# Kernel tuning notes

Measured on AMD Instinct MI355X. Metric: run time of the kernel, lower is better.

Reference implementation:

```python
import jax, jax.numpy as jnp
import numpy as np

B, N, E, H = 8, 512, 256, 8
DK = E // H
DIST_BAR = (0.3, 0.7, 1e10)  # init dist_bar + [1e10] appended in forward
NEG = -1e10


def setup_inputs() -> dict:
    key = jax.random.key(0)
    ks = jax.random.split(key, 24)
    s = 0.02
    inp = {
        'query': jax.random.normal(ks[0], (B, N, E), jnp.float32),
        'key':   jax.random.normal(ks[1], (B, N, E), jnp.float32),
        'value': jax.random.normal(ks[2], (B, N, E), jnp.float32),
        'dist':  jax.random.uniform(ks[3], (B, N, N), jnp.float32),
        'mask':  jax.random.randint(ks[4], (B, N, N), 0, 2).astype(jnp.int32),
        # 4 linears (q, k, v, out), stored as [in, out] for x @ W
        'Wq': jax.random.normal(ks[5], (E, E)) * s, 'bq': jnp.zeros((E,)),
        'Wk': jax.random.normal(ks[6], (E, E)) * s, 'bk': jnp.zeros((E,)),
        'Wv': jax.random.normal(ks[7], (E, E)) * s, 'bv': jnp.zeros((E,)),
        'Wo': jax.random.normal(ks[8], (E, E)) * s, 'bo': jnp.zeros((E,)),
        # cnn: Conv2d(1,H,1) -> ReLU -> Conv2d(H,H,1); 1x1 convs = per-pixel linear maps
        'cw1': jax.random.normal(ks[9], (H,)) * s,     'cb1': jnp.zeros((H,)),
        'cw2': jax.random.normal(ks[10], (H, H)) * s,  'cb2': jnp.zeros((H,)),
        # scale_linear: Linear(3E, E) -> ReLU -> Linear(E, E)
        'Ws1': jax.random.normal(ks[11], (3 * E, E)) * s, 'bs1': jnp.zeros((E,)),
        'Ws2': jax.random.normal(ks[12], (E, E)) * s,     'bs2': jnp.zeros((E,)),
    }
    return inp


def reference(query, key, value, dist, mask,
              Wq, bq, Wk, bk, Wv, bv, Wo, bo,
              cw1, cb1, cw2, cb2, Ws1, bs1, Ws2, bs2):
    def heads(x, W, b):  # [B,N,E] -> [B,H,N,DK]
        return (x @ W + b).reshape(B, N, H, DK).transpose(0, 2, 1, 3)

    q, k, v = heads(query, Wq, bq), heads(key, Wk, bk), heads(value, Wv, bv)
    d4 = dist[:, None]  # [B,1,N,N]
    # 1x1 conv stack: [B,1,N,N] -> [B,H,N,N]
    c1 = jax.nn.relu(d4 * cw1[None, :, None, None] + cb1[None, :, None, None])
    dist_conv = jnp.einsum('oi,bijk->bojk', cw2, c1) + cb2[None, :, None, None]

    scores = jnp.einsum('bhqd,bhkd->bhqk', q, k) / np.sqrt(DK).astype(np.float32)
    scores = scores * dist_conv
    scores = jnp.where(mask[:, None] == 0, NEG, scores)

    outs = []
    for bar in DIST_BAR:
        dm = d4 < bar                       # [B,1,N,N] bool
        dm = dm.at[:, :, 0, :].set(True).at[:, :, :, 0].set(True)
        s = jnp.where(dm, scores, NEG)
        p = jax.nn.softmax(s, axis=-1)      # [B,H,N,N]
        o = jnp.einsum('bhqk,bhkd->bhqd', p, v)
        o = o.transpose(0, 2, 1, 3).reshape(B, N, E)
        outs.append(o @ Wo + bo)
    x = jnp.concatenate(outs, axis=-1)      # [B,N,3E]
    h1 = jax.nn.relu(x @ Ws1 + bs1)
    return h1 @ Ws2 + bs2                   # [B,N,E]
```

## Files before the change

kernel.cpp:

```cpp
#include <hip/hip_runtime.h>
#include <math.h>

typedef _Float16 h16;
typedef __attribute__((ext_vector_type(4))) _Float16 h16x4;
typedef __attribute__((ext_vector_type(8))) _Float16 h16x8;
typedef __attribute__((ext_vector_type(4))) float f32x4;
typedef unsigned long long u64t;
typedef unsigned int u32t;
typedef unsigned char u8t;

__global__ __launch_bounds__(256) void prep_k(
    const float* __restrict__ Wq, const float* __restrict__ Wk,
    const float* __restrict__ Wv, const float* __restrict__ Ws2,
    const float* __restrict__ Ws1, const float* __restrict__ bo,
    const float* __restrict__ bs1,
    const float* __restrict__ cw1, const float* __restrict__ cb1,
    const float* __restrict__ cw2, const float* __restrict__ cb2,
    h16* __restrict__ WT, float* __restrict__ bcombP,
    float* __restrict__ tthr, float* __restrict__ fLUT)
{
    const int bid = blockIdx.x;
    __shared__ float T[32][33];
    if (bid < 448) {
        const int z = bid >> 6, idx = bid & 63;
        const float* in = (z == 0) ? Wq : (z == 1) ? Wk : (z == 2) ? Wv :
                          (z == 3) ? Ws2 : (Ws1 + (size_t)(z - 4) * 65536);
        h16* out = WT + (size_t)z * 65536;
        const int t = threadIdx.x, tx = t & 31, ty = t >> 5;
        const int r0 = (idx >> 3) * 32, c0 = (idx & 7) * 32;
        #pragma unroll
        for (int i = 0; i < 4; ++i)
            T[ty + i * 8][tx] = in[(size_t)(r0 + ty + i * 8) * 256 + c0 + tx];
        __syncthreads();
        #pragma unroll
        for (int i = 0; i < 4; ++i)
            out[(size_t)(c0 + ty + i * 8) * 256 + r0 + tx] = (h16)T[tx][ty + i * 8];
    } else if (bid < 464) {
        const int z = bid - 448;
        const int j = threadIdx.x;
        float acc = (z == 0) ? bs1[j] : 0.f;
        const int r0 = z * 48;
        #pragma unroll 4
        for (int r = r0; r < r0 + 48; ++r)
            acc = fmaf(bo[r & 255], Ws1[(size_t)r * 256 + j], acc);
        bcombP[z * 256 + j] = acc;
    } else {
        const int t = threadIdx.x;
        const float INVS = 0.17677669529663687f;
        float tv[8]; int zu[8];
        #pragma unroll
        for (int u = 0; u < 8; ++u) {
            const float w = cw1[u];
            zu[u] = (w == 0.f) ? 1 : 0;
            tv[u] = zu[u] ? 3.0e38f : (-cb1[u] / w);
        }
        if (t < 8) tthr[t] = tv[t];
        if (t < 72) {
            const int h = t & 7, jj = t >> 3;
            int rank[8];
            #pragma unroll
            for (int u = 0; u < 8; ++u) {
                int rk = 0;
                #pragma unroll
                for (int v = 0; v < 8; ++v)
                    rk += ((tv[v] < tv[u]) || (tv[v] == tv[u] && v < u)) ? 1 : 0;
                rank[u] = rk;
            }
            float slope = 0.f, inter = cb2[h];
            #pragma unroll
            for (int u = 0; u < 8; ++u) {
                const float c2 = cw2[h * 8 + u];
                if (zu[u]) {
                    inter += c2 * fmaxf(cb1[u], 0.f);
                } else {
                    const bool act = (cw1[u] > 0.f) ? (rank[u] < jj) : (rank[u] >= jj);
                    if (act) {
                        slope = fmaf(c2, cw1[u], slope);
                        inter = fmaf(c2, cb1[u], inter);
                    }
                }
            }
            float2 e; e.x = INVS * slope; e.y = INVS * inter;
            ((float2*)fLUT)[jj * 8 + h] = e;
        }
    }
}

__global__ __launch_bounds__(256) void qkvw_k(
    const float* __restrict__ Xq, const float* __restrict__ Xk,
    const float* __restrict__ Xv, const float* __restrict__ Wo,
    const h16* __restrict__ WT,
    const float* __restrict__ bq, const float* __restrict__ bk,
    const float* __restrict__ bv,
    h16* __restrict__ qb, h16* __restrict__ kb, h16* __restrict__ vbT,
    h16* __restrict__ WbigT)
{
    const int bid = blockIdx.x;
    const float* A; const h16* Bt; const float* bias = nullptr;
    int mode, row0, col0, sgm = 0;
    if (bid < 768) {
        const int z = bid >> 8, r = bid & 255;
        row0 = (r & 63) * 64; col0 = (r >> 6) * 64;
        A = (z == 0) ? Xq : (z == 1) ? Xk : Xv;
        Bt = WT + (size_t)z * 65536;
        bias = (z == 0) ? bq : (z == 1) ? bk : bv;
        mode = z;
    } else {
        const int r = bid - 768;
        sgm = r >> 4; const int tt = r & 15;
        row0 = (tt >> 2) * 64; col0 = (tt & 3) * 64;
        A = Wo; Bt = WT + (size_t)(4 + sgm) * 65536; mode = 3;
    }

    __shared__ __align__(16) h16 As[2][64][40];
    __shared__ __align__(16) h16 Bs[2][64][40];
    const int t = threadIdx.x, w = t >> 6, lane = t & 63;
    const int Q = lane >> 4, n = lane & 15;
    const int sr = t >> 2, sc = (t & 3) * 8;

    auto ldA = [&](int k0) -> h16x8 {
        const float* ap = A + (size_t)(row0 + sr) * 256 + k0 + sc;
        float4 f0 = *(const float4*)ap;
        float4 f1 = *(const float4*)(ap + 4);
        h16x8 hv;
        hv[0] = (h16)f0.x; hv[1] = (h16)f0.y; hv[2] = (h16)f0.z; hv[3] = (h16)f0.w;
        hv[4] = (h16)f1.x; hv[5] = (h16)f1.y; hv[6] = (h16)f1.z; hv[7] = (h16)f1.w;
        return hv;
    };
    auto ldB = [&](int k0) -> h16x8 {
        return *(const h16x8*)(Bt + (size_t)(col0 + sr) * 256 + k0 + sc);
    };

    {
        h16x8 a0 = ldA(0), b0 = ldB(0);
        *(h16x8*)&As[0][sr][sc] = a0;
        *(h16x8*)&Bs[0][sr][sc] = b0;
    }
    __syncthreads();

    f32x4 acc4[4];
    #pragma unroll
    for (int c = 0; c < 4; ++c) acc4[c] = (f32x4){0.f, 0.f, 0.f, 0.f};

    for (int it = 0; it < 8; ++it) {
        const int cur = it & 1;
        h16x8 arN, brN;
        if (it < 7) { arN = ldA(32 * (it + 1)); brN = ldB(32 * (it + 1)); }
        h16x8 af = *(const h16x8*)&As[cur][w * 16 + n][Q * 8];
        #pragma unroll
        for (int cg = 0; cg < 4; ++cg) {
            h16x8 bf = *(const h16x8*)&Bs[cur][cg * 16 + n][Q * 8];
            acc4[cg] = __builtin_amdgcn_mfma_f32_16x16x32_f16(af, bf, acc4[cg], 0, 0, 0);
        }
        if (it < 7) {
            *(h16x8*)&As[cur ^ 1][sr][sc] = arN;
            *(h16x8*)&Bs[cur ^ 1][sr][sc] = brN;
        }
        __syncthreads();
    }

    if (mode < 2) {
        h16* out = mode ? kb : qb;
        #pragma unroll
        for (int cg = 0; cg < 4; ++cg) {
            const float bvv = bias[col0 + cg * 16 + n];
            #pragma unroll
            for (int r = 0; r < 4; ++r)
                out[(size_t)(row0 + w * 16 + 4 * Q + r) * 256 + col0 + cg * 16 + n] =
                    (h16)(acc4[cg][r] + bvv);
        }
    } else if (mode == 2) {
        const int bb = row0 >> 9;
        #pragma unroll
        for (int cg = 0; cg < 4; ++cg) {
            const float bvv = bias[col0 + cg * 16 + n];
            const int col = col0 + cg * 16 + n;
            #pragma unroll
            for (int r = 0; r < 4; ++r) {
                const int m = row0 + w * 16 + 4 * Q + r;
                vbT[((size_t)(bb * 256 + col)) * 512 + (m & 511)] = (h16)(acc4[cg][r] + bvv);
            }
        }
    } else {
        #pragma unroll
        for (int cg = 0; cg < 4; ++cg) {
            const int col = col0 + cg * 16 + n;
            #pragma unroll
            for (int r = 0; r < 4; ++r)
                WbigT[(size_t)col * 768 + sgm * 256 + row0 + w * 16 + 4 * Q + r] =
                    (h16)acc4[cg][r];
        }
    }
}

template<int OUT16RELU>
__global__ __launch_bounds__(256) void hgemm32_k(
    const h16* __restrict__ A, const h16* __restrict__ Bt,
    const float* __restrict__ bias, void* __restrict__ outv, int K, int nbp)
{
    __shared__ __align__(16) h16 As[2][32][72];
    __shared__ __align__(16) h16 Bs[2][64][72];
    const int t = threadIdx.x, w = t >> 6, lane = t & 63;
    const int Q = lane >> 4, n = lane & 15;
    const int row0 = blockIdx.x * 32, col0 = blockIdx.y * 64;
    const int r16 = (w & 1) * 16, c32 = (w >> 1) * 32;
    const int asr = t >> 3, asc = (t & 7) * 8;
    const int bsr = t >> 2, bsc = (t & 3) * 16;

    auto ldA = [&](int k0) -> h16x8 {
        return *(const h16x8*)(A + (size_t)(row0 + asr) * K + k0 + asc);
    };
    auto ldB0 = [&](int k0) -> h16x8 {
        return *(const h16x8*)(Bt + (size_t)(col0 + bsr) * K + k0 + bsc);
    };
    auto ldB1 = [&](int k0) -> h16x8 {
        return *(const h16x8*)(Bt + (size_t)(col0 + bsr) * K + k0 + bsc + 8);
    };

    {
        h16x8 a0 = ldA(0), b0 = ldB0(0), b1 = ldB1(0);
        *(h16x8*)&As[0][asr][asc] = a0;
        *(h16x8*)&Bs[0][bsr][bsc] = b0;
        *(h16x8*)&Bs[0][bsr][bsc + 8] = b1;
    }
    __syncthreads();

    f32x4 acc2[2];
    acc2[0] = (f32x4){0.f, 0.f, 0.f, 0.f};
    acc2[1] = (f32x4){0.f, 0.f, 0.f, 0.f};
    const int iters = K >> 6;

    for (int it = 0; it < iters; ++it) {
        const int cur = it & 1;
        h16x8 arN, brN0, brN1;
        if (it + 1 < iters) {
            arN = ldA(64 * (it + 1));
            brN0 = ldB0(64 * (it + 1));
            brN1 = ldB1(64 * (it + 1));
        }
        #pragma unroll
        for (int kh = 0; kh < 2; ++kh) {
            h16x8 af = *(const h16x8*)&As[cur][r16 + n][kh * 32 + Q * 8];
            #pragma unroll
            for (int cg = 0; cg < 2; ++cg) {
                h16x8 bf = *(const h16x8*)&Bs[cur][c32 + cg * 16 + n][kh * 32 + Q * 8];
                acc2[cg] = __builtin_amdgcn_mfma_f32_16x16x32_f16(af, bf, acc2[cg], 0, 0, 0);
            }
        }
        if (it + 1 < iters) {
            *(h16x8*)&As[cur ^ 1][asr][asc] = arN;
            *(h16x8*)&Bs[cur ^ 1][bsr][bsc] = brN0;
            *(h16x8*)&Bs[cur ^ 1][bsr][bsc + 8] = brN1;
        }
        __syncthreads();
    }

    #pragma unroll
    for (int cg = 0; cg < 2; ++cg) {
        const int col = col0 + c32 + cg * 16 + n;
        float bv = bias[col];
        for (int p = 1; p < nbp; ++p) bv += bias[p * 256 + col];
        #pragma unroll
        for (int r = 0; r < 4; ++r) {
            const int row = row0 + r16 + 4 * Q + r;
            if (OUT16RELU)
                ((h16*)outv)[(size_t)row * 256 + col] = (h16)fmaxf(acc2[cg][r] + bv, 0.f);
            else
                ((float*)outv)[(size_t)row * 256 + col] = acc2[cg][r] + bv;
        }
    }
}

__global__ __launch_bounds__(256, 2) void attn_k(
    const h16* __restrict__ qb, const h16* __restrict__ kb,
    const h16* __restrict__ vbT,
    const float* __restrict__ dist, const int* __restrict__ mask,
    const float* __restrict__ tthr, const float* __restrict__ fLUT,
    h16* __restrict__ OB)
{
    const int bx = blockIdx.x, b = bx >> 5, q0 = (bx & 31) * 16;
    const int hg = blockIdx.y;
    const int t = threadIdx.x, w = t >> 6, lane = t & 63;
    const int Q = lane >> 4, n = lane & 15;
    const int h = hg * 4 + w;

    __shared__ __align__(16) h16 Ft[2][16][66][4];
    __shared__ __align__(16) u8t Cd[2][16][72];
    __shared__ __align__(16) h16 Sx[4][16][72];
    __shared__ __align__(8)  float2 lutS[4][9];

    float th[8];
    #pragma unroll
    for (int u = 0; u < 8; ++u) th[u] = tthr[u];
    if (t < 36) {
        const int hh = t / 9, j = t - hh * 9;
        lutS[hh][j] = ((const float2*)fLUT)[j * 8 + hg * 4 + hh];
    }
    __syncthreads();

    const h16x8 aq =
        *(const h16x8*)(qb + ((size_t)(b * 512 + q0 + n)) * 256 + h * 32 + Q * 8);

    const f32x4 z4 = {0.f, 0.f, 0.f, 0.f};
    f32x4 acc[3][2];
    #pragma unroll
    for (int s = 0; s < 3; ++s) { acc[s][0] = z4; acc[s][1] = z4; }
    float mprev = -3e38f;
    float lsum[3] = {0.f, 0.f, 0.f};

    const int scol = lane;

    auto stage = [&](int buf, int kkb, const float* dp, const int* mp) {
        #pragma unroll
        for (int i = 0; i < 4; ++i) {
            const int row = w + 4 * i;
            const float d = dp[i];
            int idx = 0;
            #pragma unroll
            for (int u = 0; u < 8; ++u) idx += (d > th[u]) ? 1 : 0;
            const bool fr = ((q0 + row) == 0) || ((kkb + scol) == 0);
            const bool keep = (mp[i] != 0);
            const u32t code = (keep && (fr || d < 0.3f) ? 1u : 0u)
                            | (keep && (fr || d < 0.7f) ? 2u : 0u)
                            | (keep ? 4u : 0u);
            Cd[buf][row][scol] = (u8t)code;
            h16x4 fv;
            #pragma unroll
            for (int hh = 0; hh < 4; ++hh) {
                const float2 si = lutS[hh][idx];
                fv[hh] = (h16)fmaf(d, si.x, si.y);
            }
            *(h16x4*)&Ft[buf][row][scol][0] = fv;
        }
    };

    float dv[4]; int mkv[4];
    #pragma unroll
    for (int i = 0; i < 4; ++i) {
        const size_t off = ((size_t)(b * 512 + q0 + w + 4 * i)) * 512 + scol;
        dv[i] = dist[off]; mkv[i] = mask[off];
    }
    h16x8 kf[4], vf[4];
    #pragma unroll
    for (int cg = 0; cg < 4; ++cg)
        kf[cg] = *(const h16x8*)(kb + ((size_t)(b * 512 + cg * 16 + n)) * 256 + h * 32 + Q * 8);
    #pragma unroll
    for (int nh = 0; nh < 2; ++nh)
        #pragma unroll
        for (int k2 = 0; k2 < 2; ++k2)
            vf[nh * 2 + k2] = *(const h16x8*)(
                vbT + ((size_t)((b * 8 + h) * 32 + nh * 16 + n)) * 512 + k2 * 32 + Q * 8);
    stage(0, 0, dv, mkv);
    __syncthreads();

    for (int kc = 0; kc < 8; ++kc) {
        const int cur = kc & 1, kk0 = kc * 64;

        float dN[4]; int mkN[4]; h16x8 kfN[4], vfN[4];
        if (kc < 7) {
            const int kn = kk0 + 64;
            #pragma unroll
            for (int i = 0; i < 4; ++i) {
                const size_t off = ((size_t)(b * 512 + q0 + w + 4 * i)) * 512 + kn + scol;
                dN[i] = dist[off]; mkN[i] = mask[off];
            }
            #pragma unroll
            for (int cg = 0; cg < 4; ++cg)
                kfN[cg] = *(const h16x8*)(
                    kb + ((size_t)(b * 512 + kn + cg * 16 + n)) * 256 + h * 32 + Q * 8);
            #pragma unroll
            for (int nh = 0; nh < 2; ++nh)
                #pragma unroll
                for (int k2 = 0; k2 < 2; ++k2)
                    vfN[nh * 2 + k2] = *(const h16x8*)(
                        vbT + ((size_t)((b * 8 + h) * 32 + nh * 16 + n)) * 512
                            + kn + k2 * 32 + Q * 8);
        }

        f32x4 s4[4];
        #pragma unroll
        for (int cg = 0; cg < 4; ++cg)
            s4[cg] = __builtin_amdgcn_mfma_f32_16x16x32_f16(aq, kf[cg], z4, 0, 0, 0);

        #pragma unroll
        for (int cg = 0; cg < 4; ++cg)
            #pragma unroll
            for (int r = 0; r < 4; ++r) {
                const float f = (float)Ft[cur][4 * Q + r][cg * 16 + n][w];
                Sx[w][4 * Q + r][cg * 16 + n] = (h16)(s4[cg][r] * f);
            }
        __builtin_amdgcn_wave_barrier();

        const u64t cd0 = *(const u64t*)&Cd[cur][n][Q * 8];
        const u64t cd1 = *(const u64t*)&Cd[cur][n][32 + Q * 8];
        float sv[16];
        {
            h16x8 s0 = *(const h16x8*)&Sx[w][n][Q * 8];
            h16x8 s1 = *(const h16x8*)&Sx[w][n][32 + Q * 8];
            #pragma unroll
            for (int j = 0; j < 8; ++j) { sv[j] = (float)s0[j]; sv[8 + j] = (float)s1[j]; }
        }
        float cm = -3e38f;
        #pragma unroll
        for (int i = 0; i < 16; ++i) {
            const u32t cc = (u32t)((i < 8 ? cd0 : cd1) >> (8 * (i & 7))) & 7u;
            cm = fmaxf(cm, (cc & 4u) ? sv[i] : -3e38f);
        }
        cm = fmaxf(cm, __shfl_xor(cm, 16));
        cm = fmaxf(cm, __shfl_xor(cm, 32));
        const float mnew = fmaxf(mprev, cm);
        const float alphaA = __expf(mprev - mnew);
        mprev = mnew;

        #pragma unroll
        for (int r = 0; r < 4; ++r) {
            const float aR = __shfl(alphaA, 4 * Q + r);
            #pragma unroll
            for (int s = 0; s < 3; ++s) { acc[s][0][r] *= aR; acc[s][1][r] *= aR; }
        }

        h16x8 pf[3][2];
        float l0 = 0.f, l1 = 0.f, l2 = 0.f;
        #pragma unroll
        for (int i = 0; i < 16; ++i) {
            const u32t cc = (u32t)((i < 8 ? cd0 : cd1) >> (8 * (i & 7))) & 7u;
            const float e = __expf(sv[i] - mnew);
            const float p0 = (cc & 1u) ? e : 0.f;
            const float p1 = (cc & 2u) ? e : 0.f;
            const float p2 = (cc & 4u) ? e : 0.f;
            l0 += p0; l1 += p1; l2 += p2;
            pf[0][i >> 3][i & 7] = (h16)p0;
            pf[1][i >> 3][i & 7] = (h16)p1;
            pf[2][i >> 3][i & 7] = (h16)p2;
        }
        lsum[0] = lsum[0] * alphaA + l0;
        lsum[1] = lsum[1] * alphaA + l1;
        lsum[2] = lsum[2] * alphaA + l2;

        #pragma unroll
        for (int k2 = 0; k2 < 2; ++k2)
            #pragma unroll
            for (int nh = 0; nh < 2; ++nh)
                #pragma unroll
                for (int s = 0; s < 3; ++s)
                    acc[s][nh] = __builtin_amdgcn_mfma_f32_16x16x32_f16(
                        pf[s][k2], vf[nh * 2 + k2], acc[s][nh], 0, 0, 0);

        if (kc < 7) {
            stage(cur ^ 1, kk0 + 64, dN, mkN);
            #pragma unroll
            for (int i = 0; i < 4; ++i) { kf[i] = kfN[i]; vf[i] = vfN[i]; dv[i] = dN[i]; mkv[i] = mkN[i]; }
        }
        __syncthreads();
    }

    float lrow[3];
    #pragma unroll
    for (int s = 0; s < 3; ++s) {
        float lv = lsum[s];
        lv += __shfl_xor(lv, 16);
        lv += __shfl_xor(lv, 32);
        lrow[s] = lv;
    }
    #pragma unroll
    for (int s = 0; s < 3; ++s) {
        #pragma unroll
        for (int r = 0; r < 4; ++r) {
            const float il = 1.0f / __shfl(lrow[s], 4 * Q + r);
            const size_t row = (size_t)(b * 512 + q0 + 4 * Q + r);
            h16* op = OB + row * 768 + s * 256 + h * 32 + n;
            op[0]  = (h16)(acc[s][0][r] * il);
            op[16] = (h16)(acc[s][1][r] * il);
        }
    }
}

extern "C" void kernel_launch(void* const* d_in, const int* in_sizes, int n_in,
                              void* d_out, int out_size, void* d_ws, size_t ws_size,
                              hipStream_t stream)
{
    const float* query = (const float*)d_in[0];
    const float* key   = (const float*)d_in[1];
    const float* value = (const float*)d_in[2];
    const float* dist  = (const float*)d_in[3];
    const int*   mask  = (const int*)d_in[4];
    const float* Wq = (const float*)d_in[5];  const float* bq = (const float*)d_in[6];
    const float* Wk = (const float*)d_in[7];  const float* bk = (const float*)d_in[8];
    const float* Wv = (const float*)d_in[9];  const float* bv = (const float*)d_in[10];
    const float* Wo = (const float*)d_in[11]; const float* bo = (const float*)d_in[12];
    const float* cw1 = (const float*)d_in[13]; const float* cb1 = (const float*)d_in[14];
    const float* cw2 = (const float*)d_in[15]; const float* cb2 = (const float*)d_in[16];
    const float* Ws1 = (const float*)d_in[17]; const float* bs1 = (const float*)d_in[18];
    const float* Ws2 = (const float*)d_in[19]; const float* bs2 = (const float*)d_in[20];

    h16* qb    = (h16*)d_ws;
    h16* kb    = qb + 1048576;
    h16* vbT   = kb + 1048576;
    h16* OB    = vbT + 1048576;
    h16* h1    = OB + 3145728;
    h16* WT    = h1 + 1048576;
    h16* WbigT = WT + 458752;
    float* bcombP = (float*)(WbigT + 196608);
    float* tthr   = bcombP + 4096;
    float* fLUT   = tthr + 8;

    prep_k<<<dim3(465), 256, 0, stream>>>(Wq, Wk, Wv, Ws2, Ws1, bo, bs1,
                                          cw1, cb1, cw2, cb2, WT, bcombP, tthr, fLUT);

    qkvw_k<<<dim3(816), 256, 0, stream>>>(query, key, value, Wo, WT,
                                          bq, bk, bv, qb, kb, vbT, WbigT);

    attn_k<<<dim3(256, 2), 256, 0, stream>>>(qb, kb, vbT, dist, mask,
                                             tthr, fLUT, OB);

    hgemm32_k<1><<<dim3(128, 4), 256, 0, stream>>>(OB, WbigT, bcombP, h1, 768, 16);
    hgemm32_k<0><<<dim3(128, 4), 256, 0, stream>>>(h1, WT + 3 * 65536, bs2, d_out, 256, 1);
}
```

Measured before the change: 166.0 us.

## Merge head groups into one 8-wave attention block and pre-convert GEMM inputs to fp16

The attention kernel now uses 512-thread blocks that cover all 8 heads, so dist and mask are loaded and staged once per query tile instead of once per head group. Shared memory holds the fp16 distance plus a LUT index packed into the code byte, and the per-head conv factor is applied at softmax time rather than staged per head. Separately, prep_k converts query/key/value/Wo to fp16 into workspace, so the QKV GEMM loads fp16 directly instead of converting fp32 on the fly. This adds an extra conversion pass over the inputs and more per-element ALU work in the softmax loop. The grid also halves to 256 blocks, which may reduce occupancy.

```diff
diff --git a/kernel.cpp b/kernel.cpp
--- a/kernel.cpp
+++ b/kernel.cpp
@@ -16,8 +16,11 @@
     const float* __restrict__ bs1,
     const float* __restrict__ cw1, const float* __restrict__ cb1,
     const float* __restrict__ cw2, const float* __restrict__ cb2,
+    const float* __restrict__ Xq, const float* __restrict__ Xk,
+    const float* __restrict__ Xv, const float* __restrict__ Wo,
     h16* __restrict__ WT, float* __restrict__ bcombP,
-    float* __restrict__ tthr, float* __restrict__ fLUT)
+    float* __restrict__ tthr, float* __restrict__ fLUT,
+    h16* __restrict__ XHx, h16* __restrict__ XHw)
 {
     const int bid = blockIdx.x;
     __shared__ float T[32][33];
@@ -44,7 +47,7 @@
         for (int r = r0; r < r0 + 48; ++r)
             acc = fmaf(bo[r & 255], Ws1[(size_t)r * 256 + j], acc);
         bcombP[z * 256 + j] = acc;
-    } else {
+    } else if (bid == 464) {
         const int t = threadIdx.x;
         const float INVS = 0.17677669529663687f;
         float tv[8]; int zu[8];
@@ -83,12 +86,28 @@
             float2 e; e.x = INVS * slope; e.y = INVS * inter;
             ((float2*)fLUT)[jj * 8 + h] = e;
         }
+    } else {
+        const size_t idx = (size_t)(bid - 465) * 2048 + (size_t)threadIdx.x * 8;
+        const float* src; h16* dst;
+        if (idx < 3145728) {
+            const int z = (int)(idx >> 20);
+            src = ((z == 0) ? Xq : (z == 1) ? Xk : Xv) + (idx & 1048575);
+            dst = XHx + idx;
+        } else {
+            src = Wo + (idx - 3145728);
+            dst = XHw + (idx - 3145728);
+        }
+        float4 f0 = *(const float4*)src;
+        float4 f1 = *(const float4*)(src + 4);
+        h16x8 hv;
+        hv[0] = (h16)f0.x; hv[1] = (h16)f0.y; hv[2] = (h16)f0.z; hv[3] = (h16)f0.w;
+        hv[4] = (h16)f1.x; hv[5] = (h16)f1.y; hv[6] = (h16)f1.z; hv[7] = (h16)f1.w;
+        *(h16x8*)dst = hv;
     }
 }
 
 __global__ __launch_bounds__(256) void qkvw_k(
-    const float* __restrict__ Xq, const float* __restrict__ Xk,
-    const float* __restrict__ Xv, const float* __restrict__ Wo,
+    const h16* __restrict__ XHx, const h16* __restrict__ XHw,
     const h16* __restrict__ WT,
     const float* __restrict__ bq, const float* __restrict__ bk,
     const float* __restrict__ bv,
@@ -96,12 +115,12 @@
     h16* __restrict__ WbigT)
 {
     const int bid = blockIdx.x;
-    const float* A; const h16* Bt; const float* bias = nullptr;
+    const h16* A; const h16* Bt; const float* bias = nullptr;
     int mode, row0, col0, sgm = 0;
     if (bid < 768) {
         const int z = bid >> 8, r = bid & 255;
         row0 = (r & 63) * 64; col0 = (r >> 6) * 64;
-        A = (z == 0) ? Xq : (z == 1) ? Xk : Xv;
+        A = XHx + (size_t)z * 1048576;
         Bt = WT + (size_t)z * 65536;
         bias = (z == 0) ? bq : (z == 1) ? bk : bv;
         mode = z;
@@ -109,7 +128,7 @@
         const int r = bid - 768;
         sgm = r >> 4; const int tt = r & 15;
         row0 = (tt >> 2) * 64; col0 = (tt & 3) * 64;
-        A = Wo; Bt = WT + (size_t)(4 + sgm) * 65536; mode = 3;
+        A = XHw; Bt = WT + (size_t)(4 + sgm) * 65536; mode = 3;
     }
 
     __shared__ __align__(16) h16 As[2][64][40];
@@ -119,13 +138,7 @@
     const int sr = t >> 2, sc = (t & 3) * 8;
 
     auto ldA = [&](int k0) -> h16x8 {
-        const float* ap = A + (size_t)(row0 + sr) * 256 + k0 + sc;
-        float4 f0 = *(const float4*)ap;
-        float4 f1 = *(const float4*)(ap + 4);
-        h16x8 hv;
-        hv[0] = (h16)f0.x; hv[1] = (h16)f0.y; hv[2] = (h16)f0.z; hv[3] = (h16)f0.w;
-        hv[4] = (h16)f1.x; hv[5] = (h16)f1.y; hv[6] = (h16)f1.z; hv[7] = (h16)f1.w;
-        return hv;
+        return *(const h16x8*)(A + (size_t)(row0 + sr) * 256 + k0 + sc);
     };
     auto ldB = [&](int k0) -> h16x8 {
         return *(const h16x8*)(Bt + (size_t)(col0 + sr) * 256 + k0 + sc);
@@ -271,7 +284,7 @@
     }
 }
 
-__global__ __launch_bounds__(256, 2) void attn_k(
+__global__ __launch_bounds__(512, 2) void attn_k(
     const h16* __restrict__ qb, const h16* __restrict__ kb,
     const h16* __restrict__ vbT,
     const float* __restrict__ dist, const int* __restrict__ mask,
@@ -279,24 +292,19 @@
     h16* __restrict__ OB)
 {
     const int bx = blockIdx.x, b = bx >> 5, q0 = (bx & 31) * 16;
-    const int hg = blockIdx.y;
     const int t = threadIdx.x, w = t >> 6, lane = t & 63;
     const int Q = lane >> 4, n = lane & 15;
-    const int h = hg * 4 + w;
-
-    __shared__ __align__(16) h16 Ft[2][16][66][4];
+    const int h = w;
+
+    __shared__ __align__(16) h16 Dd[2][16][72];
     __shared__ __align__(16) u8t Cd[2][16][72];
-    __shared__ __align__(16) h16 Sx[4][16][72];
-    __shared__ __align__(8)  float2 lutS[4][9];
+    __shared__ __align__(16) h16 Sx[8][16][72];
+    __shared__ __align__(8)  float2 lutS[8][9];
 
     float th[8];
     #pragma unroll
     for (int u = 0; u < 8; ++u) th[u] = tthr[u];
-    if (t < 36) {
-        const int hh = t / 9, j = t - hh * 9;
-        lutS[hh][j] = ((const float2*)fLUT)[j * 8 + hg * 4 + hh];
-    }
-    __syncthreads();
+    if (t < 72) lutS[t & 7][t >> 3] = ((const float2*)fLUT)[t];
 
     const h16x8 aq =
         *(const h16x8*)(qb + ((size_t)(b * 512 + q0 + n)) * 256 + h * 32 + Q * 8);
@@ -312,8 +320,8 @@
 
     auto stage = [&](int buf, int kkb, const float* dp, const int* mp) {
         #pragma unroll
-        for (int i = 0; i < 4; ++i) {
-            const int row = w + 4 * i;
+        for (int i = 0; i < 2; ++i) {
+            const int row = w + 8 * i;
             const float d = dp[i];
             int idx = 0;
             #pragma unroll
@@ -322,22 +330,17 @@
             const bool keep = (mp[i] != 0);
             const u32t code = (keep && (fr || d < 0.3f) ? 1u : 0u)
                             | (keep && (fr || d < 0.7f) ? 2u : 0u)
-                            | (keep ? 4u : 0u);
+                            | (keep ? 4u : 0u)
+                            | ((u32t)idx << 3);
             Cd[buf][row][scol] = (u8t)code;
-            h16x4 fv;
-            #pragma unroll
-            for (int hh = 0; hh < 4; ++hh) {
-                const float2 si = lutS[hh][idx];
-                fv[hh] = (h16)fmaf(d, si.x, si.y);
-            }
-            *(h16x4*)&Ft[buf][row][scol][0] = fv;
+            Dd[buf][row][scol] = (h16)d;
         }
     };
 
-    float dv[4]; int mkv[4];
-    #pragma unroll
-    for (int i = 0; i < 4; ++i) {
-        const size_t off = ((size_t)(b * 512 + q0 + w + 4 * i)) * 512 + scol;
+    float dv[2]; int mkv[2];
+    #pragma unroll
+    for (int i = 0; i < 2; ++i) {
+        const size_t off = ((size_t)(b * 512 + q0 + w + 8 * i)) * 512 + scol;
         dv[i] = dist[off]; mkv[i] = mask[off];
     }
     h16x8 kf[4], vf[4];
@@ -356,12 +359,12 @@
     for (int kc = 0; kc < 8; ++kc) {
         const int cur = kc & 1, kk0 = kc * 64;
 
-        float dN[4]; int mkN[4]; h16x8 kfN[4], vfN[4];
+        float dN[2]; int mkN[2]; h16x8 kfN[4], vfN[4];
         if (kc < 7) {
             const int kn = kk0 + 64;
             #pragma unroll
-            for (int i = 0; i < 4; ++i) {
-                const size_t off = ((size_t)(b * 512 + q0 + w + 4 * i)) * 512 + kn + scol;
+            for (int i = 0; i < 2; ++i) {
+                const size_t off = ((size_t)(b * 512 + q0 + w + 8 * i)) * 512 + kn + scol;
                 dN[i] = dist[off]; mkN[i] = mask[off];
             }
             #pragma unroll
@@ -385,20 +388,27 @@
         #pragma unroll
         for (int cg = 0; cg < 4; ++cg)
             #pragma unroll
-            for (int r = 0; r < 4; ++r) {
-                const float f = (float)Ft[cur][4 * Q + r][cg * 16 + n][w];
-                Sx[w][4 * Q + r][cg * 16 + n] = (h16)(s4[cg][r] * f);
-            }
+            for (int r = 0; r < 4; ++r)
+                Sx[w][4 * Q + r][cg * 16 + n] = (h16)s4[cg][r];
         __builtin_amdgcn_wave_barrier();
 
         const u64t cd0 = *(const u64t*)&Cd[cur][n][Q * 8];
         const u64t cd1 = *(const u64t*)&Cd[cur][n][32 + Q * 8];
+        const h16x8 dd0 = *(const h16x8*)&Dd[cur][n][Q * 8];
+        const h16x8 dd1 = *(const h16x8*)&Dd[cur][n][32 + Q * 8];
         float sv[16];
         {
             h16x8 s0 = *(const h16x8*)&Sx[w][n][Q * 8];
             h16x8 s1 = *(const h16x8*)&Sx[w][n][32 + Q * 8];
             #pragma unroll
-            for (int j = 0; j < 8; ++j) { sv[j] = (float)s0[j]; sv[8 + j] = (float)s1[j]; }
+            for (int i = 0; i < 16; ++i) {
+                const u32t byte = (u32t)((i < 8 ? cd0 : cd1) >> (8 * (i & 7))) & 0xFFu;
+                const int idx = (int)(byte >> 3);
+                const float2 se = lutS[w][idx];
+                const float dfi = (float)((i < 8) ? dd0[i & 7] : dd1[i & 7]);
+                const float f = fmaf(dfi, se.x, se.y);
+                sv[i] = (float)((i < 8) ? s0[i & 7] : s1[i & 7]) * f;
+            }
         }
         float cm = -3e38f;
         #pragma unroll
@@ -449,7 +459,7 @@
         if (kc < 7) {
             stage(cur ^ 1, kk0 + 64, dN, mkN);
             #pragma unroll
-            for (int i = 0; i < 4; ++i) { kf[i] = kfN[i]; vf[i] = vfN[i]; dv[i] = dN[i]; mkv[i] = mkN[i]; }
+            for (int i = 0; i < 4; ++i) { kf[i] = kfN[i]; vf[i] = vfN[i]; }
         }
         __syncthreads();
     }
@@ -500,18 +510,21 @@
     h16* h1    = OB + 3145728;
     h16* WT    = h1 + 1048576;
     h16* WbigT = WT + 458752;
-    float* bcombP = (float*)(WbigT + 196608);
+    h16* XHw   = WbigT + 196608;
+    float* bcombP = (float*)(XHw + 65536);
     float* tthr   = bcombP + 4096;
     float* fLUT   = tthr + 8;
-
-    prep_k<<<dim3(465), 256, 0, stream>>>(Wq, Wk, Wv, Ws2, Ws1, bo, bs1,
-                                          cw1, cb1, cw2, cb2, WT, bcombP, tthr, fLUT);
-
-    qkvw_k<<<dim3(816), 256, 0, stream>>>(query, key, value, Wo, WT,
-                                          bq, bk, bv, qb, kb, vbT, WbigT);
-
-    attn_k<<<dim3(256, 2), 256, 0, stream>>>(qb, kb, vbT, dist, mask,
-                                             tthr, fLUT, OB);
+    h16* XHx   = OB;
+
+    prep_k<<<dim3(2033), 256, 0, stream>>>(Wq, Wk, Wv, Ws2, Ws1, bo, bs1,
+                                           cw1, cb1, cw2, cb2,
+                                           query, key, value, Wo,
+                                           WT, bcombP, tthr, fLUT, XHx, XHw);
+
+    qkvw_k<<<dim3(816), 256, 0, stream>>>(XHx, XHw, WT, bq, bk, bv, qb, kb, vbT, WbigT);
+
+    attn_k<<<dim3(256), 512, 0, stream>>>(qb, kb, vbT, dist, mask,
+                                          tthr, fLUT, OB);
 
     hgemm32_k<1><<<dim3(128, 4), 256, 0, stream>>>(OB, WbigT, bcombP, h1, 768, 16);
     hgemm32_k<0><<<dim3(128, 4), 256, 0, stream>>>(h1, WT + 3 * 65536, bs2, d_out, 256, 1);
```

New measurement: 160.4 us. -3.4%, faster.
